# Kernel optimization log

Hardware: AMD Instinct MI355X
Metric: run time of the kernel (lower is better)

Reference implementation:

```python
import jax, jax.numpy as jnp
import numpy as np

NEG = -1e9

def setup_inputs() -> dict:
    key = jax.random.key(0)
    k1, k2, k3, k4, k5 = jax.random.split(key, 5)
    B, S, D = 32, 4096, 1024
    query = jax.random.normal(k1, (B, D), dtype=jnp.float32)
    keys = jax.random.normal(k2, (B, S, D), dtype=jnp.float32)
    values = jax.random.normal(k3, (B, S, D), dtype=jnp.float32)
    mask = jax.random.randint(k4, (B, S), 0, 2, dtype=jnp.int32)
    W_q = jax.random.normal(k5, (D, D), dtype=jnp.float32) * (1.0 / np.sqrt(D))
    return {"query": query, "keys": keys, "values": values, "mask": mask, "W_q": W_q}

def reference(query, keys, values, mask, W_q):
    # q = query @ W_q.T  (nn.Linear with weight of shape [key_dim, query_dim])
    q = jnp.einsum("bq,kq->bk", query, W_q)              # (B, key_dim)
    energies = jnp.einsum("bsk,bk->bs", keys, q)          # (B, S)
    energies = jnp.where(mask == 0, NEG, energies)
    attn = jax.nn.softmax(energies, axis=1)               # (B, S)
    context = jnp.einsum("bs,bsv->bv", attn, values)      # (B, value_dim)
    return (context, attn)
```

## Files before the change

kernel.cpp:

```cpp
#include <hip/hip_runtime.h>

#define NEG_INF_E (-1e9f)

typedef float floatx4 __attribute__((ext_vector_type(4)));

__device__ __forceinline__ float wave_sum(float v) {
#pragma unroll
    for (int off = 32; off > 0; off >>= 1)
        v += __shfl_xor(v, off, 64);
    return v;
}

__device__ __forceinline__ floatx4 ntload4(const float* p) {
    return __builtin_nontemporal_load((const floatx4*)p);
}

__global__ void k_linear(const float* __restrict__ query,
                         const float* __restrict__ Wq,
                         float* __restrict__ q_out) {
    const int lane = threadIdx.x & 63;
    const int wid  = blockIdx.x * 4 + (threadIdx.x >> 6);
    const int b = wid >> 10;
    const int k = wid & 1023;
    const floatx4* qr = (const floatx4*)(query + (size_t)b * 1024);
    const floatx4* wr = (const floatx4*)(Wq + (size_t)k * 1024);
    float acc = 0.f;
#pragma unroll
    for (int it = 0; it < 4; ++it) {
        floatx4 a = qr[lane + it * 64];
        floatx4 w = wr[lane + it * 64];
        acc += a.x * w.x + a.y * w.y + a.z * w.z + a.w * w.w;
    }
    acc = wave_sum(acc);
    if (lane == 0) q_out[(size_t)b * 1024 + k] = acc;
}

__global__ void k_energy(const float* __restrict__ keys,
                         const float* __restrict__ q,
                         const int* __restrict__ mask,
                         float* __restrict__ energies) {
    const int lane = threadIdx.x & 63;
    const int wid  = blockIdx.x * 4 + (threadIdx.x >> 6);
    const int b = wid >> 12;
    const float* kr = keys + (size_t)wid * 1024;
    const floatx4* qr = (const floatx4*)(q + (size_t)b * 1024);
    floatx4 kv[4], qv[4];
#pragma unroll
    for (int it = 0; it < 4; ++it) kv[it] = ntload4(kr + (lane + it * 64) * 4);
#pragma unroll
    for (int it = 0; it < 4; ++it) qv[it] = qr[lane + it * 64];
    float acc = 0.f;
#pragma unroll
    for (int it = 0; it < 4; ++it) {
        acc += kv[it].x * qv[it].x + kv[it].y * qv[it].y +
               kv[it].z * qv[it].z + kv[it].w * qv[it].w;
    }
    acc = wave_sum(acc);
    if (lane == 0)
        energies[wid] = (mask[wid] == 0) ? NEG_INF_E : acc;
}

__global__ void k_softmax(float* __restrict__ d_out) {
    __shared__ float red[16];
    const int b = blockIdx.x;
    const int tid = threadIdx.x;
    const int lane = tid & 63;
    const int wv = tid >> 6;

    d_out[(size_t)b * 1024 + tid] = 0.f;

    float* e = d_out + 32768 + (size_t)b * 4096;
    float v[4];
    float m = -INFINITY;
#pragma unroll
    for (int i = 0; i < 4; ++i) {
        v[i] = e[tid + i * 1024];
        m = fmaxf(m, v[i]);
    }
#pragma unroll
    for (int off = 32; off > 0; off >>= 1)
        m = fmaxf(m, __shfl_xor(m, off, 64));
    if (lane == 0) red[wv] = m;
    __syncthreads();
    float bm = red[0];
#pragma unroll
    for (int i = 1; i < 16; ++i) bm = fmaxf(bm, red[i]);
    __syncthreads();

    float s = 0.f;
#pragma unroll
    for (int i = 0; i < 4; ++i) {
        v[i] = expf(v[i] - bm);
        s += v[i];
    }
    s = wave_sum(s);
    if (lane == 0) red[wv] = s;
    __syncthreads();
    float bs = 0.f;
#pragma unroll
    for (int i = 0; i < 16; ++i) bs += red[i];
    const float inv = 1.f / bs;
#pragma unroll
    for (int i = 0; i < 4; ++i) e[tid + i * 1024] = v[i] * inv;
}

__global__ void k_context(const float* __restrict__ values,
                          const float* __restrict__ attn,
                          float* __restrict__ context) {
    __shared__ float a_s[128];
    const int b = blockIdx.x;
    const int s0 = blockIdx.y * 128;
    const int tid = threadIdx.x;

    if (tid < 128) a_s[tid] = attn[(size_t)b * 4096 + s0 + tid];
    __syncthreads();

    const float* vr = values + ((size_t)b * 4096 + s0) * 1024;
    floatx4 acc = (floatx4)0.f;
#pragma unroll 8
    for (int s = 0; s < 128; ++s) {
        const float a = a_s[s];
        const floatx4 v = ntload4(vr + (size_t)s * 1024 + tid * 4);
        acc.x += a * v.x;
        acc.y += a * v.y;
        acc.z += a * v.z;
        acc.w += a * v.w;
    }
    float* c = context + (size_t)b * 1024 + tid * 4;
    atomicAdd(c + 0, acc.x);
    atomicAdd(c + 1, acc.y);
    atomicAdd(c + 2, acc.z);
    atomicAdd(c + 3, acc.w);
}

extern "C" void kernel_launch(void* const* d_in, const int* in_sizes, int n_in,
                              void* d_out, int out_size, void* d_ws, size_t ws_size,
                              hipStream_t stream) {
    const float* query  = (const float*)d_in[0];
    const float* keys   = (const float*)d_in[1];
    const float* values = (const float*)d_in[2];
    const int*   mask   = (const int*)d_in[3];
    const float* Wq     = (const float*)d_in[4];
    float* out = (float*)d_out;

    float* q_tmp    = out;
    float* energies = out + 32768;

    k_linear<<<8192, 256, 0, stream>>>(query, Wq, q_tmp);
    k_energy<<<32768, 256, 0, stream>>>(keys, q_tmp, mask, energies);
    k_softmax<<<32, 1024, 0, stream>>>(out);
    k_context<<<dim3(32, 32), 256, 0, stream>>>(values, energies, out);
}
```

Measured before the change: 183.8 us.

## Fuse softmax into context kernel using workspace for energies

Stores q and energies in workspace and drops the separate softmax launch. Every context block recomputes the row max and sum over all 4096 energies, normalises its own 128-element slice, writes it to the attn output and uses it for the weighted sum of values. Zeroing of the context output moves into the linear kernel. This removes one launch and a serialized 32-block softmax pass, at the cost of redundant reduction work in each of the 1024 context blocks. It only applies when the workspace is large enough.

```diff
diff --git a/kernel.cpp b/kernel.cpp
--- a/kernel.cpp
+++ b/kernel.cpp
@@ -11,17 +11,28 @@
     return v;
 }
 
+__device__ __forceinline__ float wave_max(float v) {
+#pragma unroll
+    for (int off = 32; off > 0; off >>= 1)
+        v = fmaxf(v, __shfl_xor(v, off, 64));
+    return v;
+}
+
 __device__ __forceinline__ floatx4 ntload4(const float* p) {
     return __builtin_nontemporal_load((const floatx4*)p);
 }
 
+template <bool ZERO_CTX>
 __global__ void k_linear(const float* __restrict__ query,
                          const float* __restrict__ Wq,
-                         float* __restrict__ q_out) {
+                         float* __restrict__ q_out,
+                         float* __restrict__ ctx_zero) {
     const int lane = threadIdx.x & 63;
     const int wid  = blockIdx.x * 4 + (threadIdx.x >> 6);
     const int b = wid >> 10;
     const int k = wid & 1023;
+    if (ZERO_CTX && blockIdx.x < 128)
+        ctx_zero[blockIdx.x * 256 + threadIdx.x] = 0.f;
     const floatx4* qr = (const floatx4*)(query + (size_t)b * 1024);
     const floatx4* wr = (const floatx4*)(Wq + (size_t)k * 1024);
     float acc = 0.f;
@@ -60,6 +71,64 @@
         energies[wid] = (mask[wid] == 0) ? NEG_INF_E : acc;
 }
 
+__global__ void k_context_fused(const float* __restrict__ values,
+                                const float* __restrict__ energies,
+                                float* __restrict__ out) {
+    __shared__ float red[4];
+    __shared__ float a_s[128];
+    const int b = blockIdx.x;
+    const int s0 = blockIdx.y * 128;
+    const int tid = threadIdx.x;
+    const int lane = tid & 63;
+    const int wv = tid >> 6;
+
+    const float* e = energies + (size_t)b * 4096;
+    float ev[16];
+    float m = -INFINITY;
+#pragma unroll
+    for (int i = 0; i < 16; ++i) {
+        ev[i] = e[tid + i * 256];
+        m = fmaxf(m, ev[i]);
+    }
+    m = wave_max(m);
+    if (lane == 0) red[wv] = m;
+    __syncthreads();
+    const float bm = fmaxf(fmaxf(red[0], red[1]), fmaxf(red[2], red[3]));
+    __syncthreads();
+
+    float s = 0.f;
+#pragma unroll
+    for (int i = 0; i < 16; ++i) s += expf(ev[i] - bm);
+    s = wave_sum(s);
+    if (lane == 0) red[wv] = s;
+    __syncthreads();
+    const float inv = 1.f / (red[0] + red[1] + red[2] + red[3]);
+
+    if (tid < 128) {
+        const float a = expf(e[s0 + tid] - bm) * inv;
+        a_s[tid] = a;
+        __builtin_nontemporal_store(a, out + 32768 + (size_t)b * 4096 + s0 + tid);
+    }
+    __syncthreads();
+
+    const float* vr = values + ((size_t)b * 4096 + s0) * 1024;
+    floatx4 acc = (floatx4)0.f;
+#pragma unroll 8
+    for (int s2 = 0; s2 < 128; ++s2) {
+        const float a = a_s[s2];
+        const floatx4 v = ntload4(vr + (size_t)s2 * 1024 + tid * 4);
+        acc.x += a * v.x;
+        acc.y += a * v.y;
+        acc.z += a * v.z;
+        acc.w += a * v.w;
+    }
+    float* c = out + (size_t)b * 1024 + tid * 4;
+    atomicAdd(c + 0, acc.x);
+    atomicAdd(c + 1, acc.y);
+    atomicAdd(c + 2, acc.z);
+    atomicAdd(c + 3, acc.w);
+}
+
 __global__ void k_softmax(float* __restrict__ d_out) {
     __shared__ float red[16];
     const int b = blockIdx.x;
@@ -77,9 +146,7 @@
         v[i] = e[tid + i * 1024];
         m = fmaxf(m, v[i]);
     }
-#pragma unroll
-    for (int off = 32; off > 0; off >>= 1)
-        m = fmaxf(m, __shfl_xor(m, off, 64));
+    m = wave_max(m);
     if (lane == 0) red[wv] = m;
     __syncthreads();
     float bm = red[0];
@@ -143,11 +210,18 @@
     const float* Wq     = (const float*)d_in[4];
     float* out = (float*)d_out;
 
-    float* q_tmp    = out;
-    float* energies = out + 32768;
-
-    k_linear<<<8192, 256, 0, stream>>>(query, Wq, q_tmp);
-    k_energy<<<32768, 256, 0, stream>>>(keys, q_tmp, mask, energies);
-    k_softmax<<<32, 1024, 0, stream>>>(out);
-    k_context<<<dim3(32, 32), 256, 0, stream>>>(values, energies, out);
-}
+    if (ws_size >= (32768 + 131072) * sizeof(float)) {
+        float* q_tmp    = (float*)d_ws;
+        float* energies = (float*)d_ws + 32768;
+        k_linear<true><<<8192, 256, 0, stream>>>(query, Wq, q_tmp, out);
+        k_energy<<<32768, 256, 0, stream>>>(keys, q_tmp, mask, energies);
+        k_context_fused<<<dim3(32, 32), 256, 0, stream>>>(values, energies, out);
+    } else {
+        float* q_tmp    = out;
+        float* energies = out + 32768;
+        k_linear<false><<<8192, 256, 0, stream>>>(query, Wq, q_tmp, out);
+        k_energy<<<32768, 256, 0, stream>>>(keys, q_tmp, mask, energies);
+        k_softmax<<<32, 1024, 0, stream>>>(out);
+        k_context<<<dim3(32, 32), 256, 0, stream>>>(values, energies, out);
+    }
+}
```

Result: no change. 182.4 us (median of 2 runs) (-0.8%).
